# Optimization experiments

Measured on AMD Instinct MI355X. Metric: run time of the kernel, lower is better.

## Reference

```python
import jax, jax.numpy as jnp
import numpy as np
from jax.scipy.stats import norm

B, S, D, E, K = 16, 512, 768, 16, 4
NOISE_EPS = 0.01
LOSS_COEF = 0.01


def setup_inputs() -> dict:
    key = jax.random.key(0)
    ks = jax.random.split(key, 6)
    x = jax.random.normal(ks[0], (B, S, D), dtype=jnp.float32)
    noise = jax.random.normal(ks[1], (B, E), dtype=jnp.float32)
    w_gate = jax.random.normal(ks[2], (D, E), dtype=jnp.float32) * 0.02
    w_noise = jax.random.normal(ks[3], (D, E), dtype=jnp.float32) * 0.02
    # initialize_sInit: log(1/(n_experts-1))
    sparse_threshold = jnp.full((1, 1), np.log(1.0 / (E - 1)), dtype=jnp.float32)
    weight = jax.random.normal(ks[4], (E, D, D), dtype=jnp.float32) * 0.02
    bias = jax.random.normal(ks[5], (E, D), dtype=jnp.float32) * 0.02
    return {"x": x, "noise": noise, "w_gate": w_gate, "w_noise": w_noise,
            "sparse_threshold": sparse_threshold, "weight": weight, "bias": bias}


def _cv_squared(v):
    v = v.astype(jnp.float32)
    return jnp.var(v, ddof=1) / (jnp.mean(v) ** 2 + 1e-10)


def reference(x, noise, w_gate, w_noise, sparse_threshold, weight, bias):
    # ---- str_gating (training path, noise supplied externally) ----
    xm = x.mean(axis=1)                                 # [B, D]
    clean_logits = xm @ w_gate                          # [B, E]
    noise_stddev = jax.nn.softplus(xm @ w_noise) + NOISE_EPS
    noisy_logits = clean_logits + noise * noise_stddev  # [B, E]
    gates = jax.nn.softmax(noisy_logits, axis=1)
    # sparseFunction: sign(g) * relu(|g| - sigmoid(s))
    gates = jnp.sign(gates) * jax.nn.relu(jnp.abs(gates) - jax.nn.sigmoid(sparse_threshold))
    # ---- load via _prob_in_top_k (k < n_experts, noisy gating, train) ----
    top_vals = jax.lax.top_k(noisy_logits, K + 1)[0]    # [B, K+1]
    thr_in = top_vals[:, K:K + 1]                       # (k+1)-th largest
    thr_out = top_vals[:, K - 1:K]                      # k-th largest
    is_in = noisy_logits > thr_in
    prob_in = norm.cdf((clean_logits - thr_in) / noise_stddev)
    prob_out = norm.cdf((clean_logits - thr_out) / noise_stddev)
    load = jnp.where(is_in, prob_in, prob_out).sum(axis=0)   # [E]
    importance = gates.sum(axis=0)                      # [E]
    loss = (_cv_squared(importance) + _cv_squared(load)) * LOSS_COEF
    # ---- per-example expert weight mixing (torch broadcasts [B,E,O,I]; same math) ----
    expert_weights = jnp.einsum('be,eoi->boi', gates, weight)  # [B, O, I]
    expert_bias = jnp.einsum('be,eo->bo', gates, bias)         # [B, O]
    # ---- batched matmul: einsum('bij,bkj->bik') ----
    y = jnp.einsum('bsi,boi->bso', x, expert_weights) + expert_bias[:, None, :]
    return y, loss
```

## Files before the change

kernel.cpp:

```cpp
#include <hip/hip_runtime.h>
#include <hip/hip_bf16.h>

#define B_ 16
#define S_ 512
#define D_ 768
#define E_ 16
#define K_ 4

typedef __attribute__((ext_vector_type(8))) short short8;
typedef __attribute__((ext_vector_type(4))) float f32x4;

#define GLOAD16(gp, lp)                                             \
    __builtin_amdgcn_global_load_lds(                               \
        (const __attribute__((address_space(1))) void*)(gp),        \
        (__attribute__((address_space(3))) void*)(lp), 16, 0, 0)

__global__ void k1_mean_cvt(const float* __restrict__ x, __hip_bfloat16* __restrict__ xb,
                            float* __restrict__ partial) {
    int t  = threadIdx.x;
    int b  = blockIdx.x;
    int sc = blockIdx.y;
    size_t rowbase = ((size_t)b * S_ + (size_t)sc * 32) * D_ + t * 4;

    float4 acc = make_float4(0.f, 0.f, 0.f, 0.f);
    #pragma unroll 8
    for (int s = 0; s < 32; ++s) {
        float4 v = *(const float4*)(x + rowbase + (size_t)s * D_);
        acc.x += v.x; acc.y += v.y; acc.z += v.z; acc.w += v.w;
        __hip_bfloat16 h0 = __float2bfloat16(v.x);
        __hip_bfloat16 h1 = __float2bfloat16(v.y);
        __hip_bfloat16 h2 = __float2bfloat16(v.z);
        __hip_bfloat16 h3 = __float2bfloat16(v.w);
        ushort4 pk;
        pk.x = *(unsigned short*)&h0; pk.y = *(unsigned short*)&h1;
        pk.z = *(unsigned short*)&h2; pk.w = *(unsigned short*)&h3;
        *(ushort4*)((unsigned short*)xb + rowbase + (size_t)s * D_) = pk;
    }
    *(float4*)(partial + ((size_t)sc * B_ + b) * D_ + t * 4) = acc;
}

__global__ void k2a_logits(const float* __restrict__ partial,
                           const float* __restrict__ noise,
                           const float* __restrict__ w_gate,
                           const float* __restrict__ w_noise,
                           const float* __restrict__ thr_ptr,
                           float* __restrict__ gates_out,
                           float* __restrict__ clean_out,
                           float* __restrict__ std_out,
                           float* __restrict__ noisy_out,
                           float* __restrict__ thrin_out,
                           float* __restrict__ throut_out) {
    __shared__ float xm[D_];
    __shared__ float red[2][16][17];
    __shared__ float s_noisy[E_];

    int b = blockIdx.x, t = threadIdx.x;

    for (int d = t; d < D_; d += 256) {
        float s = 0.f;
        #pragma unroll
        for (int c = 0; c < 16; ++c) s += partial[((size_t)c * B_ + b) * D_ + d];
        xm[d] = s * (1.0f / S_);
    }
    __syncthreads();

    int e = t & 15, sl = t >> 4;
    const float* wg = w_gate  + (size_t)sl * 48 * E_ + e;
    const float* wn = w_noise + (size_t)sl * 48 * E_ + e;
    float cl = 0.f, nz = 0.f;
    #pragma unroll
    for (int i = 0; i < 48; ++i) {
        float xv = xm[sl * 48 + i];
        cl += xv * wg[(size_t)i * E_];
        nz += xv * wn[(size_t)i * E_];
    }
    red[0][sl][e] = cl;
    red[1][sl][e] = nz;
    __syncthreads();

    if (t < E_) {
        float c2 = 0.f, n2 = 0.f;
        #pragma unroll
        for (int s2 = 0; s2 < 16; ++s2) { c2 += red[0][s2][t]; n2 += red[1][s2][t]; }
        float sp     = fmaxf(n2, 0.f) + log1pf(expf(-fabsf(n2)));
        float stddev = sp + 0.01f;
        float ny     = c2 + noise[b * E_ + t] * stddev;
        s_noisy[t] = ny;
        clean_out[b * E_ + t] = c2;
        std_out[b * E_ + t]   = stddev;
        noisy_out[b * E_ + t] = ny;
    }
    __syncthreads();

    if (t < E_) {
        float ny = s_noisy[t];
        int rank = 0;
        #pragma unroll
        for (int j = 0; j < E_; ++j) {
            float vj = s_noisy[j];
            if (vj > ny || (vj == ny && j < t)) rank++;
        }
        if (rank == K_)     thrin_out[b]  = ny;
        if (rank == K_ - 1) throut_out[b] = ny;

        float mx = -1e30f;
        #pragma unroll
        for (int j = 0; j < E_; ++j) mx = fmaxf(mx, s_noisy[j]);
        float den = 0.f;
        #pragma unroll
        for (int j = 0; j < E_; ++j) den += expf(s_noisy[j] - mx);
        float gate = expf(ny - mx) / den;
        float sig  = 1.f / (1.f + expf(-thr_ptr[0]));
        gates_out[b * E_ + t] = fmaxf(gate - sig, 0.f);
    }
}

__global__ void k3_wb(const float* __restrict__ gates, const float* __restrict__ weight,
                      const float* __restrict__ bias,
                      const float* __restrict__ clean,
                      const float* __restrict__ stdv,
                      const float* __restrict__ noisyv,
                      const float* __restrict__ thrin,
                      const float* __restrict__ throut,
                      __hip_bfloat16* __restrict__ wb, float* __restrict__ ebias,
                      float* __restrict__ loss_out) {
    __shared__ float g[B_ * E_];
    int t = threadIdx.x;
    g[t] = gates[t];
    __syncthreads();

    if (blockIdx.x == 624) {
        __shared__ float s_imp[E_], s_load[E_];
        if (t < E_) {
            float imp = 0.f, ld = 0.f;
            #pragma unroll
            for (int bb = 0; bb < B_; ++bb) {
                imp += g[bb * E_ + t];
                float ti = thrin[bb], to = throut[bb];
                float c2 = clean[bb * E_ + t], sd = stdv[bb * E_ + t], nl = noisyv[bb * E_ + t];
                float z  = (nl > ti) ? (c2 - ti) / sd : (c2 - to) / sd;
                ld += 0.5f * erfcf(-z * 0.70710678118654752f);
            }
            s_imp[t]  = imp;
            s_load[t] = ld;
        }
        __syncthreads();
        if (t == 0) {
            float m1 = 0.f, m2 = 0.f;
            #pragma unroll
            for (int j = 0; j < E_; ++j) { m1 += s_imp[j]; m2 += s_load[j]; }
            m1 /= E_; m2 /= E_;
            float v1 = 0.f, v2 = 0.f;
            #pragma unroll
            for (int j = 0; j < E_; ++j) {
                float a = s_imp[j]  - m1; v1 += a * a;
                float c = s_load[j] - m2; v2 += c * c;
            }
            v1 /= (E_ - 1); v2 /= (E_ - 1);
            loss_out[0] = (v1 / (m1 * m1 + 1e-10f) + v2 / (m2 * m2 + 1e-10f)) * 0.01f;
        }
        return;
    }

    if (blockIdx.x >= 576) {
        int idx = (blockIdx.x - 576) * 256 + t;
        int b = idx / D_, o = idx % D_;
        float acc = 0.f;
        #pragma unroll
        for (int e = 0; e < E_; ++e) acc += g[b * E_ + e] * bias[e * D_ + o];
        ebias[idx] = acc;
        return;
    }

    size_t base = ((size_t)blockIdx.x * 256 + t) * 4;
    float4 acc[B_];
    #pragma unroll
    for (int b = 0; b < B_; ++b) acc[b] = make_float4(0.f, 0.f, 0.f, 0.f);

    #pragma unroll
    for (int e = 0; e < E_; ++e) {
        float4 w4 = *(const float4*)(weight + (size_t)e * D_ * D_ + base);
        #pragma unroll
        for (int b = 0; b < B_; ++b) {
            float ge = g[b * E_ + e];
            acc[b].x += ge * w4.x; acc[b].y += ge * w4.y;
            acc[b].z += ge * w4.z; acc[b].w += ge * w4.w;
        }
    }
    #pragma unroll
    for (int b = 0; b < B_; ++b) {
        __hip_bfloat16 h0 = __float2bfloat16(acc[b].x);
        __hip_bfloat16 h1 = __float2bfloat16(acc[b].y);
        __hip_bfloat16 h2 = __float2bfloat16(acc[b].z);
        __hip_bfloat16 h3 = __float2bfloat16(acc[b].w);
        ushort4 pk;
        pk.x = *(unsigned short*)&h0; pk.y = *(unsigned short*)&h1;
        pk.z = *(unsigned short*)&h2; pk.w = *(unsigned short*)&h3;
        *(ushort4*)((unsigned short*)wb + (size_t)b * D_ * D_ + base) = pk;
    }
}

#define BM 128
#define BN 96
#define BK 64
#define NT (D_ / BK)

__global__ __launch_bounds__(256, 2) void k4_gemm(const __hip_bfloat16* __restrict__ xb,
                                                  const __hip_bfloat16* __restrict__ wbm,
                                                  const float* __restrict__ ebias,
                                                  float* __restrict__ y) {
    __shared__ __hip_bfloat16 As[2][BM][BK];
    __shared__ __hip_bfloat16 Bs[2][BN][BK];

    int t = threadIdx.x;
    int wgid  = blockIdx.x;
    int xcd   = wgid & 7;
    int local = wgid >> 3;
    int b  = (xcd << 1) | (local & 1);
    int r2 = local >> 1;
    int bm = r2 & 3;
    int bn = r2 >> 2;

    const __hip_bfloat16* xp = xb  + (size_t)b * S_ * D_ + (size_t)(bm * BM) * D_;
    const __hip_bfloat16* wp = wbm + (size_t)b * D_ * D_ + (size_t)(bn * BN) * D_;

    int wave = t >> 6, lane = t & 63;
    int wm = wave >> 1, wn = wave & 1;
    int lrow = lane & 15;
    int lk   = (lane >> 4) << 3;
    int swz  = (lrow & 7) << 3;

    int lr  = lane >> 3;
    int lcs = (((lane & 7) ^ lr) << 3);

    f32x4 zero4 = {0.f, 0.f, 0.f, 0.f};
    f32x4 acc[4][3];
    #pragma unroll
    for (int m = 0; m < 4; ++m)
        #pragma unroll
        for (int n = 0; n < 3; ++n) acc[m][n] = zero4;

    #define STAGE(buf, k0)                                                          \
        do {                                                                        \
            _Pragma("unroll")                                                       \
            for (int i = 0; i < 4; ++i) {                                           \
                int r = wave * 32 + i * 8;                                          \
                GLOAD16(xp + (size_t)(r + lr) * D_ + (k0) + lcs, &As[buf][r][0]);   \
            }                                                                       \
            _Pragma("unroll")                                                       \
            for (int i = 0; i < 3; ++i) {                                           \
                int r = wave * 24 + i * 8;                                          \
                GLOAD16(wp + (size_t)(r + lr) * D_ + (k0) + lcs, &Bs[buf][r][0]);   \
            }                                                                       \
        } while (0)

    #define COMPUTE(buf)                                                            \
        do {                                                                        \
            _Pragma("unroll")                                                       \
            for (int kk = 0; kk < BK; kk += 32) {                                   \
                short8 afr[4], bfr[3];                                              \
                _Pragma("unroll")                                                   \
                for (int m = 0; m < 4; ++m)                                         \
                    afr[m] = *(const short8*)(&As[buf][wm * 64 + m * 16 + lrow]     \
                                                 [(kk + lk) ^ swz]);                \
                _Pragma("unroll")                                                   \
                for (int n = 0; n < 3; ++n)                                         \
                    bfr[n] = *(const short8*)(&Bs[buf][wn * 48 + n * 16 + lrow]     \
                                                 [(kk + lk) ^ swz]);                \
                _Pragma("unroll")                                                   \
                for (int m = 0; m < 4; ++m)                                         \
                    _Pragma("unroll")                                               \
                    for (int n = 0; n < 3; ++n)                                     \
                        acc[m][n] = __builtin_amdgcn_mfma_f32_16x16x32_bf16(        \
                            afr[m], bfr[n], acc[m][n], 0, 0, 0);                    \
            }                                                                       \
        } while (0)

    STAGE(0, 0);
    __syncthreads();
    int cur = 0;
    for (int kt = 0; kt < NT - 1; ++kt) {
        STAGE(cur ^ 1, (kt + 1) * BK);
        COMPUTE(cur);
        __syncthreads();
        cur ^= 1;
    }
    COMPUTE(cur);

    float* yp = y + (size_t)b * S_ * D_ + (size_t)(bm * BM) * D_ + bn * BN;
    const float* ep = ebias + (size_t)b * D_ + bn * BN;
    int crow = (lane >> 4) * 4;
    int ccol = lane & 15;
    #pragma unroll
    for (int n = 0; n < 3; ++n) {
        float eb = ep[wn * 48 + n * 16 + ccol];
        #pragma unroll
        for (int m = 0; m < 4; ++m) {
            #pragma unroll
            for (int j = 0; j < 4; ++j) {
                __builtin_nontemporal_store(acc[m][n][j] + eb,
                    yp + (size_t)(wm * 64 + m * 16 + crow + j) * D_ + wn * 48 + n * 16 + ccol);
            }
        }
    }
    #undef STAGE
    #undef COMPUTE
}

extern "C" void kernel_launch(void* const* d_in, const int* in_sizes, int n_in,
                              void* d_out, int out_size, void* d_ws, size_t ws_size,
                              hipStream_t stream) {
    const float* x       = (const float*)d_in[0];
    const float* noise   = (const float*)d_in[1];
    const float* w_gate  = (const float*)d_in[2];
    const float* w_noise = (const float*)d_in[3];
    const float* thr     = (const float*)d_in[4];
    const float* weight  = (const float*)d_in[5];
    const float* bias    = (const float*)d_in[6];
    float* out = (float*)d_out;

    char* ws = (char*)d_ws;
    float*          partial = (float*)(ws + 0);
    float*          gates   = (float*)(ws + 786432);
    float*          clean   = (float*)(ws + 787456);
    float*          stdv    = (float*)(ws + 788480);
    float*          noisyv  = (float*)(ws + 789504);
    float*          thrin   = (float*)(ws + 790528);
    float*          throut  = (float*)(ws + 790592);
    float*          ebias   = (float*)(ws + 790656);
    __hip_bfloat16* xb      = (__hip_bfloat16*)(ws + 839808);
    __hip_bfloat16* wb      = (__hip_bfloat16*)(ws + 13422720);

    k1_mean_cvt<<<dim3(B_, 16), 192, 0, stream>>>(x, xb, partial);
    k2a_logits<<<16, 256, 0, stream>>>(partial, noise, w_gate, w_noise, thr, gates,
                                       clean, stdv, noisyv, thrin, throut);
    k3_wb<<<625, 256, 0, stream>>>(gates, weight, bias, clean, stdv, noisyv, thrin, throut,
                                   wb, ebias, out + (size_t)B_ * S_ * D_);
    k4_gemm<<<512, 256, 0, stream>>>(xb, wb, ebias, out);
}
```

Baseline: 58.10 us.

## Fuse gating and loss into conversion kernel via last-block atomic counter

Merges the mean/convert kernel with the gating-logits kernel using a global atomic counter: the last of the 256 blocks to finish reduces the partial means and computes logits, gates, top-k thresholds and the auxiliary loss for all batches in one block. The loss computation also moves out of the weight-mixing kernel, which removes one launch and the intermediate clean/std/noisy buffers. The tail work now runs serially on a single 192-thread block. The counter relies on wrap-around modulo 256 and is never reset, so correctness across repeated calls depends on that arithmetic. A stray redefined GLOAD16 macro is left in, but it is immediately undefined.

New measurement: 99.73 us. 1.72x slower.

```diff
diff --git a/kernel.cpp b/kernel.cpp
--- a/kernel.cpp
+++ b/kernel.cpp
@@ -11,12 +11,23 @@
 typedef __attribute__((ext_vector_type(4))) float f32x4;
 
 #define GLOAD16(gp, lp)                                             \
+    __builtin_amdgcn_global_lds_impl(gp, lp)
+#undef GLOAD16
+#define GLOAD16(gp, lp)                                             \
     __builtin_amdgcn_global_load_lds(                               \
         (const __attribute__((address_space(1))) void*)(gp),        \
         (__attribute__((address_space(3))) void*)(lp), 16, 0, 0)
 
-__global__ void k1_mean_cvt(const float* __restrict__ x, __hip_bfloat16* __restrict__ xb,
-                            float* __restrict__ partial) {
+__global__ void kA_cvt_gate(const float* __restrict__ x,
+                            const float* __restrict__ noise,
+                            const float* __restrict__ w_gate,
+                            const float* __restrict__ w_noise,
+                            const float* __restrict__ thr_ptr,
+                            __hip_bfloat16* __restrict__ xb,
+                            float* __restrict__ partial,
+                            float* __restrict__ gates_g,
+                            float* __restrict__ loss_out,
+                            unsigned int* __restrict__ cnt) {
     int t  = threadIdx.x;
     int b  = blockIdx.x;
     int sc = blockIdx.y;
@@ -37,130 +48,132 @@
         *(ushort4*)((unsigned short*)xb + rowbase + (size_t)s * D_) = pk;
     }
     *(float4*)(partial + ((size_t)sc * B_ + b) * D_ + t * 4) = acc;
-}
-
-__global__ void k2a_logits(const float* __restrict__ partial,
-                           const float* __restrict__ noise,
-                           const float* __restrict__ w_gate,
-                           const float* __restrict__ w_noise,
-                           const float* __restrict__ thr_ptr,
-                           float* __restrict__ gates_out,
-                           float* __restrict__ clean_out,
-                           float* __restrict__ std_out,
-                           float* __restrict__ noisy_out,
-                           float* __restrict__ thrin_out,
-                           float* __restrict__ throut_out) {
-    __shared__ float xm[D_];
-    __shared__ float red[2][16][17];
-    __shared__ float s_noisy[E_];
-
-    int b = blockIdx.x, t = threadIdx.x;
-
-    for (int d = t; d < D_; d += 256) {
-        float s = 0.f;
-        #pragma unroll
-        for (int c = 0; c < 16; ++c) s += partial[((size_t)c * B_ + b) * D_ + d];
-        xm[d] = s * (1.0f / S_);
-    }
-    __syncthreads();
-
-    int e = t & 15, sl = t >> 4;
-    const float* wg = w_gate  + (size_t)sl * 48 * E_ + e;
-    const float* wn = w_noise + (size_t)sl * 48 * E_ + e;
-    float cl = 0.f, nz = 0.f;
-    #pragma unroll
-    for (int i = 0; i < 48; ++i) {
-        float xv = xm[sl * 48 + i];
-        cl += xv * wg[(size_t)i * E_];
-        nz += xv * wn[(size_t)i * E_];
-    }
-    red[0][sl][e] = cl;
-    red[1][sl][e] = nz;
-    __syncthreads();
-
-    if (t < E_) {
+
+    __threadfence();
+    __shared__ unsigned int s_old;
+    if (t == 0) s_old = atomicAdd(cnt, 1u);
+    __syncthreads();
+    if ((s_old & 255u) != 255u) return;
+    __threadfence();
+
+    __shared__ float xmT[D_ * B_ / 4][4];
+    #define XMT(d, bb) xmT[((d) * B_ + (bb)) >> 2][((d) * B_ + (bb)) & 3]
+    __shared__ float redc[12][E_][B_], redn[12][E_][B_];
+    __shared__ float s_noisy[B_][E_ + 1], s_clean[B_][E_ + 1], s_std[B_][E_ + 1];
+    __shared__ float thrin_s[B_], throut_s[B_];
+    __shared__ float gsl[B_][E_], s_imp[E_], s_load[E_];
+
+    for (int j = t; j < 3072; j += 192) {
+        int bb = j / 192, d4 = j % 192;
+        f32x4 s = {0.f, 0.f, 0.f, 0.f};
+        #pragma unroll
+        for (int c = 0; c < 16; ++c)
+            s += *(const f32x4*)(partial + ((size_t)c * B_ + bb) * D_ + d4 * 4);
+        #pragma unroll
+        for (int k2 = 0; k2 < 4; ++k2) XMT(d4 * 4 + k2, bb) = s[k2] * (1.0f / S_);
+    }
+    __syncthreads();
+
+    {
+        int e = t & 15, sl = t >> 4;
+        f32x4 cl0 = {0,0,0,0}, cl1 = {0,0,0,0}, cl2 = {0,0,0,0}, cl3 = {0,0,0,0};
+        f32x4 nz0 = {0,0,0,0}, nz1 = {0,0,0,0}, nz2 = {0,0,0,0}, nz3 = {0,0,0,0};
+        #pragma unroll 8
+        for (int i = 0; i < 64; ++i) {
+            int d = sl * 64 + i;
+            float wgv = w_gate [d * E_ + e];
+            float wnv = w_noise[d * E_ + e];
+            f32x4 x0 = *(const f32x4*)&XMT(d, 0);
+            f32x4 x1 = *(const f32x4*)&XMT(d, 4);
+            f32x4 x2 = *(const f32x4*)&XMT(d, 8);
+            f32x4 x3 = *(const f32x4*)&XMT(d, 12);
+            cl0 += x0 * wgv; cl1 += x1 * wgv; cl2 += x2 * wgv; cl3 += x3 * wgv;
+            nz0 += x0 * wnv; nz1 += x1 * wnv; nz2 += x2 * wnv; nz3 += x3 * wnv;
+        }
+        *(f32x4*)&redc[sl][e][0]  = cl0; *(f32x4*)&redc[sl][e][4]  = cl1;
+        *(f32x4*)&redc[sl][e][8]  = cl2; *(f32x4*)&redc[sl][e][12] = cl3;
+        *(f32x4*)&redn[sl][e][0]  = nz0; *(f32x4*)&redn[sl][e][4]  = nz1;
+        *(f32x4*)&redn[sl][e][8]  = nz2; *(f32x4*)&redn[sl][e][12] = nz3;
+    }
+    __syncthreads();
+
+    for (int idx = t; idx < B_ * E_; idx += 192) {
+        int bb = idx >> 4, e = idx & 15;
         float c2 = 0.f, n2 = 0.f;
         #pragma unroll
-        for (int s2 = 0; s2 < 16; ++s2) { c2 += red[0][s2][t]; n2 += red[1][s2][t]; }
+        for (int sl = 0; sl < 12; ++sl) { c2 += redc[sl][e][bb]; n2 += redn[sl][e][bb]; }
         float sp     = fmaxf(n2, 0.f) + log1pf(expf(-fabsf(n2)));
         float stddev = sp + 0.01f;
-        float ny     = c2 + noise[b * E_ + t] * stddev;
-        s_noisy[t] = ny;
-        clean_out[b * E_ + t] = c2;
-        std_out[b * E_ + t]   = stddev;
-        noisy_out[b * E_ + t] = ny;
+        float ny     = c2 + noise[bb * E_ + e] * stddev;
+        s_clean[bb][e] = c2;
+        s_std[bb][e]   = stddev;
+        s_noisy[bb][e] = ny;
+    }
+    __syncthreads();
+
+    float sig = 1.f / (1.f + expf(-thr_ptr[0]));
+    for (int idx = t; idx < B_ * E_; idx += 192) {
+        int bb = idx >> 4, e = idx & 15;
+        float ny = s_noisy[bb][e];
+        int rank = 0;
+        #pragma unroll
+        for (int j = 0; j < E_; ++j) {
+            float vj = s_noisy[bb][j];
+            if (vj > ny || (vj == ny && j < e)) rank++;
+        }
+        if (rank == K_)     thrin_s[bb]  = ny;
+        if (rank == K_ - 1) throut_s[bb] = ny;
+        float mx = -1e30f;
+        #pragma unroll
+        for (int j = 0; j < E_; ++j) mx = fmaxf(mx, s_noisy[bb][j]);
+        float den = 0.f;
+        #pragma unroll
+        for (int j = 0; j < E_; ++j) den += expf(s_noisy[bb][j] - mx);
+        float gate = expf(ny - mx) / den;
+        float sg   = fmaxf(gate - sig, 0.f);
+        gsl[bb][e] = sg;
+        gates_g[idx] = sg;
     }
     __syncthreads();
 
     if (t < E_) {
-        float ny = s_noisy[t];
-        int rank = 0;
+        float imp = 0.f, ld = 0.f;
+        #pragma unroll
+        for (int bb = 0; bb < B_; ++bb) {
+            imp += gsl[bb][t];
+            float ti = thrin_s[bb], to = throut_s[bb];
+            float c2 = s_clean[bb][t], sd = s_std[bb][t], nl = s_noisy[bb][t];
+            float z  = (nl > ti) ? (c2 - ti) / sd : (c2 - to) / sd;
+            ld += 0.5f * erfcf(-z * 0.70710678118654752f);
+        }
+        s_imp[t]  = imp;
+        s_load[t] = ld;
+    }
+    __syncthreads();
+    if (t == 0) {
+        float m1 = 0.f, m2 = 0.f;
+        #pragma unroll
+        for (int j = 0; j < E_; ++j) { m1 += s_imp[j]; m2 += s_load[j]; }
+        m1 /= E_; m2 /= E_;
+        float v1 = 0.f, v2 = 0.f;
         #pragma unroll
         for (int j = 0; j < E_; ++j) {
-            float vj = s_noisy[j];
-            if (vj > ny || (vj == ny && j < t)) rank++;
-        }
-        if (rank == K_)     thrin_out[b]  = ny;
-        if (rank == K_ - 1) throut_out[b] = ny;
-
-        float mx = -1e30f;
-        #pragma unroll
-        for (int j = 0; j < E_; ++j) mx = fmaxf(mx, s_noisy[j]);
-        float den = 0.f;
-        #pragma unroll
-        for (int j = 0; j < E_; ++j) den += expf(s_noisy[j] - mx);
-        float gate = expf(ny - mx) / den;
-        float sig  = 1.f / (1.f + expf(-thr_ptr[0]));
-        gates_out[b * E_ + t] = fmaxf(gate - sig, 0.f);
-    }
+            float a = s_imp[j]  - m1; v1 += a * a;
+            float c = s_load[j] - m2; v2 += c * c;
+        }
+        v1 /= (E_ - 1); v2 /= (E_ - 1);
+        loss_out[0] = (v1 / (m1 * m1 + 1e-10f) + v2 / (m2 * m2 + 1e-10f)) * 0.01f;
+    }
+    #undef XMT
 }
 
-__global__ void k3_wb(const float* __restrict__ gates, const float* __restrict__ weight,
-                      const float* __restrict__ bias,
-                      const float* __restrict__ clean,
-                      const float* __restrict__ stdv,
-                      const float* __restrict__ noisyv,
-                      const float* __restrict__ thrin,
-                      const float* __restrict__ throut,
-                      __hip_bfloat16* __restrict__ wb, float* __restrict__ ebias,
-                      float* __restrict__ loss_out) {
+__global__ void kB_mix(const float* __restrict__ gates, const float* __restrict__ weight,
+                       const float* __restrict__ bias,
+                       __hip_bfloat16* __restrict__ wb, float* __restrict__ ebias) {
     __shared__ float g[B_ * E_];
     int t = threadIdx.x;
     g[t] = gates[t];
     __syncthreads();
-
-    if (blockIdx.x == 624) {
-        __shared__ float s_imp[E_], s_load[E_];
-        if (t < E_) {
-            float imp = 0.f, ld = 0.f;
-            #pragma unroll
-            for (int bb = 0; bb < B_; ++bb) {
-                imp += g[bb * E_ + t];
-                float ti = thrin[bb], to = throut[bb];
-                float c2 = clean[bb * E_ + t], sd = stdv[bb * E_ + t], nl = noisyv[bb * E_ + t];
-                float z  = (nl > ti) ? (c2 - ti) / sd : (c2 - to) / sd;
-                ld += 0.5f * erfcf(-z * 0.70710678118654752f);
-            }
-            s_imp[t]  = imp;
-            s_load[t] = ld;
-        }
-        __syncthreads();
-        if (t == 0) {
-            float m1 = 0.f, m2 = 0.f;
-            #pragma unroll
-            for (int j = 0; j < E_; ++j) { m1 += s_imp[j]; m2 += s_load[j]; }
-            m1 /= E_; m2 /= E_;
-            float v1 = 0.f, v2 = 0.f;
-            #pragma unroll
-            for (int j = 0; j < E_; ++j) {
-                float a = s_imp[j]  - m1; v1 += a * a;
-                float c = s_load[j] - m2; v2 += c * c;
-            }
-            v1 /= (E_ - 1); v2 /= (E_ - 1);
-            loss_out[0] = (v1 / (m1 * m1 + 1e-10f) + v2 / (m2 * m2 + 1e-10f)) * 0.01f;
-        }
-        return;
-    }
 
     if (blockIdx.x >= 576) {
         int idx = (blockIdx.x - 576) * 256 + t;
@@ -205,7 +218,7 @@
 #define BK 64
 #define NT (D_ / BK)
 
-__global__ __launch_bounds__(256, 2) void k4_gemm(const __hip_bfloat16* __restrict__ xb,
+__global__ __launch_bounds__(256, 2) void kC_gemm(const __hip_bfloat16* __restrict__ xb,
                                                   const __hip_bfloat16* __restrict__ wbm,
                                                   const float* __restrict__ ebias,
                                                   float* __restrict__ y) {
@@ -322,19 +335,14 @@
     char* ws = (char*)d_ws;
     float*          partial = (float*)(ws + 0);
     float*          gates   = (float*)(ws + 786432);
-    float*          clean   = (float*)(ws + 787456);
-    float*          stdv    = (float*)(ws + 788480);
-    float*          noisyv  = (float*)(ws + 789504);
-    float*          thrin   = (float*)(ws + 790528);
-    float*          throut  = (float*)(ws + 790592);
-    float*          ebias   = (float*)(ws + 790656);
+    float*          ebias   = (float*)(ws + 787456);
     __hip_bfloat16* xb      = (__hip_bfloat16*)(ws + 839808);
     __hip_bfloat16* wb      = (__hip_bfloat16*)(ws + 13422720);
-
-    k1_mean_cvt<<<dim3(B_, 16), 192, 0, stream>>>(x, xb, partial);
-    k2a_logits<<<16, 256, 0, stream>>>(partial, noise, w_gate, w_noise, thr, gates,
-                                       clean, stdv, noisyv, thrin, throut);
-    k3_wb<<<625, 256, 0, stream>>>(gates, weight, bias, clean, stdv, noisyv, thrin, throut,
-                                   wb, ebias, out + (size_t)B_ * S_ * D_);
-    k4_gemm<<<512, 256, 0, stream>>>(xb, wb, ebias, out);
+    unsigned int*   cnt     = (unsigned int*)(ws + 32297088);
+
+    kA_cvt_gate<<<dim3(B_, 16), 192, 0, stream>>>(x, noise, w_gate, w_noise, thr,
+                                                  xb, partial, gates,
+                                                  out + (size_t)B_ * S_ * D_, cnt);
+    kB_mix<<<624, 256, 0, stream>>>(gates, weight, bias, wb, ebias);
+    kC_gemm<<<512, 256, 0, stream>>>(xb, wb, ebias, out);
 }
```
